# Kernel tuning notes

Hardware: AMD Instinct MI355X
Metric: run time of the kernel (lower is better)

## Reference

```python
import jax, jax.numpy as jnp
import numpy as np

NUM_NODES = 100000
EMB = 64
HID = 128
OUT = 64
N_EDGES = 1600000
N_LABEL = 200000


def setup_inputs() -> dict:
    key = jax.random.key(0)
    ks = jax.random.split(key, 8)
    return {
        "emb": jax.random.normal(ks[0], (NUM_NODES, EMB), jnp.float32) * 0.05,
        "w1l": jax.random.normal(ks[1], (HID, EMB), jnp.float32) * 0.05,
        "w1r": jax.random.normal(ks[2], (HID, EMB), jnp.float32) * 0.05,
        "b1": jnp.zeros((HID,), jnp.float32),
        "w2l": jax.random.normal(ks[3], (OUT, HID), jnp.float32) * 0.05,
        "w2r": jax.random.normal(ks[4], (OUT, HID), jnp.float32) * 0.05,
        "b2": jnp.zeros((OUT,), jnp.float32),
        "edge_index": jax.random.randint(ks[5], (2, N_EDGES), 0, NUM_NODES, jnp.int32),
        "edge_label_index": jax.random.randint(ks[6], (2, N_LABEL), 0, NUM_NODES, jnp.int32),
    }


def reference(emb, w1l, w1r, b1, w2l, w2r, b2, edge_index, edge_label_index):
    # PyG SAGEConv (aggr='mean'): out = mean_{j in N(i)} x_j @ W_l^T + b_l + x_i @ W_r^T
    n = emb.shape[0]
    src, dst = edge_index[0], edge_index[1]
    # in-degree per destination node, clamped to avoid div-by-zero (isolated nodes -> 0 agg)
    deg = jax.ops.segment_sum(jnp.ones(src.shape, emb.dtype), dst, num_segments=n)
    inv_deg = 1.0 / jnp.maximum(deg, 1.0)

    def sage(x, wl, wr, b):
        agg = jax.ops.segment_sum(x[src], dst, num_segments=n) * inv_deg[:, None]
        return agg @ wl.T + x @ wr.T + b

    h = jax.nn.relu(sage(emb, w1l, w1r, b1))  # dropout is identity in eval mode
    z = sage(h, w2l, w2r, b2)  # [N, OUT]
    # dot-product decode over candidate pairs
    return jnp.sum(z[edge_label_index[0]] * z[edge_label_index[1]], axis=-1)
```

## Files before the change

### kernel.cpp

```cpp
#include <hip/hip_runtime.h>

#define NN   100000
#define EMB  64
#define HID  128
#define OUTD 64
#define NE   1600000
#define NL   200000
#define NBUK 6250
#define NG   8
#define CAPG 128
#define BSTR 6272

#define BUK_BLOCKS  1563
#define CEMB_BLOCKS 400
#define CW_BLOCKS   64

typedef __attribute__((ext_vector_type(4))) float f32x4;
typedef __attribute__((ext_vector_type(8))) short s16x8;
typedef __attribute__((ext_vector_type(4))) unsigned short us4;
typedef __attribute__((ext_vector_type(4))) int v4i;

__device__ __forceinline__ unsigned short f2bf(float f) {
    unsigned u = __float_as_uint(f);
    u += 0x7FFFu + ((u >> 16) & 1u);
    return (unsigned short)(u >> 16);
}
__device__ __forceinline__ float bf2f(unsigned short h) {
    return __uint_as_float(((unsigned)h) << 16);
}

__device__ __forceinline__ unsigned xcc_id() {
    unsigned v;
    asm volatile("s_getreg_b32 %0, hwreg(HW_REG_XCC_ID)" : "=s"(v));
    return v & (NG - 1);
}

__global__ void __launch_bounds__(256) prep_kernel(
        const int* __restrict__ src, const int* __restrict__ dst,
        int* __restrict__ bcnt, int* __restrict__ tmp,
        const float* __restrict__ emb, unsigned short* __restrict__ embb,
        const float* __restrict__ w1l, const float* __restrict__ w1r,
        const float* __restrict__ w2l, const float* __restrict__ w2r,
        unsigned short* __restrict__ w1cat, unsigned short* __restrict__ w2cat) {
    const int bid = blockIdx.x;
    const int tid = threadIdx.x;

    if (bid < BUK_BLOCKS) {
        int i = bid * 256 + tid;
        if (i >= NE / 4) return;
        unsigned g = xcc_id();
        int* cb = bcnt + g * BSTR;
        v4i d4 = __builtin_nontemporal_load((const v4i*)dst + i);
        v4i s4 = __builtin_nontemporal_load((const v4i*)src + i);
        int b0 = d4[0] >> 4, b1 = d4[1] >> 4, b2 = d4[2] >> 4, b3 = d4[3] >> 4;
        int p0 = atomicAdd(&cb[b0], 1);
        int p1 = atomicAdd(&cb[b1], 1);
        int p2 = atomicAdd(&cb[b2], 1);
        int p3 = atomicAdd(&cb[b3], 1);
        if (p0 < CAPG) tmp[((size_t)g * NBUK + b0) * CAPG + p0] = ((d4[0] & 15) << 17) | s4[0];
        if (p1 < CAPG) tmp[((size_t)g * NBUK + b1) * CAPG + p1] = ((d4[1] & 15) << 17) | s4[1];
        if (p2 < CAPG) tmp[((size_t)g * NBUK + b2) * CAPG + p2] = ((d4[2] & 15) << 17) | s4[2];
        if (p3 < CAPG) tmp[((size_t)g * NBUK + b3) * CAPG + p3] = ((d4[3] & 15) << 17) | s4[3];
    } else if (bid < BUK_BLOCKS + CEMB_BLOCKS) {
        for (int i = (bid - BUK_BLOCKS) * 256 + tid; i < NN * 16; i += CEMB_BLOCKS * 256) {
            float4 v = ((const float4*)emb)[i];
            us4 o;
            o.x = f2bf(v.x); o.y = f2bf(v.y); o.z = f2bf(v.z); o.w = f2bf(v.w);
            ((us4*)embb)[i] = o;
        }
    } else {
        int t = (bid - BUK_BLOCKS - CEMB_BLOCKS) * 256 + tid;
        if (t >= 128 * 128) return;
        int o = t >> 7, k = t & 127;
        w1cat[t] = f2bf(k < 64 ? w1l[o * 64 + k] : w1r[o * 64 + (k - 64)]);
        w2cat[t] = f2bf(o < 64 ? w2l[o * 128 + k] : w2r[(o - 64) * 128 + k]);
    }
}

template<bool L1>
__global__ void __launch_bounds__(256) agg16_kernel(
        const int* __restrict__ bcnt, const int* __restrict__ tmp,
        const unsigned short* __restrict__ xb,
        const float* __restrict__ hz, const float* __restrict__ bias,
        unsigned short* __restrict__ outb) {
    __shared__ int cgs[NG];
    __shared__ int goff[NG];
    __shared__ int total;
    __shared__ int scnt[16];
    __shared__ int soff[16];
    __shared__ int scur[16];
    __shared__ int plist[NG * CAPG];
    __shared__ int slist[NG * CAPG];

    const int b    = blockIdx.x;
    const int tid  = threadIdx.x;
    const int lane = tid & 63;
    const int wv   = tid >> 6;

    if (tid < NG) cgs[tid] = min(bcnt[tid * BSTR + b], CAPG);
    if (tid < 16) scnt[tid] = 0;
    __syncthreads();

    if (tid == 0) {
        int acc = 0;
#pragma unroll
        for (int g = 0; g < NG; ++g) { int c = cgs[g]; goff[g] = acc; acc += c; }
        total = acc;
    }
    __syncthreads();

    for (int t = tid; t < NG * CAPG; t += 256) {
        int g = t >> 7;
        int i = t & (CAPG - 1);
        if (i < cgs[g])
            plist[goff[g] + i] = __builtin_nontemporal_load(
                tmp + ((size_t)g * NBUK + b) * CAPG + i);
    }
    __syncthreads();

    const int cnt = total;
    for (int i = tid; i < cnt; i += 256)
        atomicAdd(&scnt[plist[i] >> 17], 1);
    __syncthreads();

    if (tid == 0) {
        int acc = 0;
#pragma unroll
        for (int r = 0; r < 16; ++r) {
            soff[r] = acc;
            scur[r] = acc;
            acc += scnt[r];
        }
    }
    __syncthreads();

    for (int i = tid; i < cnt; i += 256) {
        int p = plist[i];
        int pos = atomicAdd(&scur[p >> 17], 1);
        slist[pos] = p & 0x1FFFF;
    }
    __syncthreads();

#define LDX(c) bf2f(xb[(size_t)(c) * 64 + lane])
    for (int r = wv; r < 16; r += 4) {
        const int node = b * 16 + r;
        const int s = soff[r];
        const int d = scnt[r];
        float acc = 0.f;
        int j = 0;
        for (; j + 8 <= d; j += 8) {
            int c0 = slist[s + j + 0], c1 = slist[s + j + 1];
            int c2 = slist[s + j + 2], c3 = slist[s + j + 3];
            int c4 = slist[s + j + 4], c5 = slist[s + j + 5];
            int c6 = slist[s + j + 6], c7 = slist[s + j + 7];
            float v0 = LDX(c0), v1 = LDX(c1), v2 = LDX(c2), v3 = LDX(c3);
            float v4 = LDX(c4), v5 = LDX(c5), v6 = LDX(c6), v7 = LDX(c7);
            acc += ((v0 + v1) + (v2 + v3)) + ((v4 + v5) + (v6 + v7));
        }
        if (j + 4 <= d) {
            int c0 = slist[s + j + 0], c1 = slist[s + j + 1];
            int c2 = slist[s + j + 2], c3 = slist[s + j + 3];
            float v0 = LDX(c0), v1 = LDX(c1), v2 = LDX(c2), v3 = LDX(c3);
            acc += (v0 + v1) + (v2 + v3);
            j += 4;
        }
        for (; j < d; ++j) acc += LDX(slist[s + j]);

        const float inv = 1.0f / fmaxf((float)d, 1.0f);
        if (L1) {
            outb[(size_t)node * 64 + lane] = f2bf(acc * inv);
        } else {
            outb[(size_t)node * 64 + lane] =
                f2bf(acc * inv + hz[(size_t)node * 64 + lane] + bias[lane]);
        }
    }
#undef LDX
}

__global__ void __launch_bounds__(256) gemm_mfma_kernel(
        const unsigned short* __restrict__ aggb, const unsigned short* __restrict__ embb,
        const unsigned short* __restrict__ w1cat, const float* __restrict__ b1,
        const unsigned short* __restrict__ w2cat,
        unsigned short* __restrict__ p2b, float* __restrict__ hz) {
    __shared__ unsigned short h_lds[128 * 136];

    const int tid  = threadIdx.x;
    const int lane = tid & 63;
    const int w    = tid >> 6;
    const int l15  = lane & 15;
    const int lk   = lane >> 4;
    const int n_base = blockIdx.x * 128;
    const int mrow0  = w * 32;

    f32x4 acc[2][8];
#pragma unroll
    for (int mt = 0; mt < 2; ++mt)
#pragma unroll
        for (int nt = 0; nt < 8; ++nt) acc[mt][nt] = (f32x4)(0.f);

#pragma unroll
    for (int ks = 0; ks < 4; ++ks) {
        const int kc = ks * 32 + lk * 8;
        s16x8 a[2];
#pragma unroll
        for (int mt = 0; mt < 2; ++mt) {
            int n = n_base + mrow0 + mt * 16 + l15;
            s16x8 av = (s16x8)(short)0;
            if (n < NN) {
                const unsigned short* ap = (kc < 64)
                    ? (aggb + (size_t)n * 64 + kc)
                    : (embb + (size_t)n * 64 + (kc - 64));
                av = *(const s16x8*)ap;
            }
            a[mt] = av;
        }
#pragma unroll
        for (int nt = 0; nt < 8; ++nt) {
            s16x8 bv = *(const s16x8*)(w1cat + (nt * 16 + l15) * 128 + kc);
            acc[0][nt] = __builtin_amdgcn_mfma_f32_16x16x32_bf16(a[0], bv, acc[0][nt], 0, 0, 0);
            acc[1][nt] = __builtin_amdgcn_mfma_f32_16x16x32_bf16(a[1], bv, acc[1][nt], 0, 0, 0);
        }
    }

    float b1v[8];
#pragma unroll
    for (int nt = 0; nt < 8; ++nt) b1v[nt] = b1[nt * 16 + l15];
#pragma unroll
    for (int mt = 0; mt < 2; ++mt)
#pragma unroll
        for (int nt = 0; nt < 8; ++nt) {
            f32x4 d = acc[mt][nt];
            int o = nt * 16 + l15;
            int r0 = mrow0 + mt * 16 + lk * 4;
#pragma unroll
            for (int j = 0; j < 4; ++j)
                h_lds[(r0 + j) * 136 + o] = f2bf(fmaxf(d[j] + b1v[nt], 0.f));
        }

#pragma unroll
    for (int mt = 0; mt < 2; ++mt)
#pragma unroll
        for (int nt = 0; nt < 8; ++nt) acc[mt][nt] = (f32x4)(0.f);

#pragma unroll
    for (int ks = 0; ks < 4; ++ks) {
        const int kc = ks * 32 + lk * 8;
        s16x8 a[2];
#pragma unroll
        for (int mt = 0; mt < 2; ++mt)
            a[mt] = *(const s16x8*)&h_lds[(mrow0 + mt * 16 + l15) * 136 + kc];
#pragma unroll
        for (int nt = 0; nt < 8; ++nt) {
            s16x8 bv = *(const s16x8*)(w2cat + (nt * 16 + l15) * 128 + kc);
            acc[0][nt] = __builtin_amdgcn_mfma_f32_16x16x32_bf16(a[0], bv, acc[0][nt], 0, 0, 0);
            acc[1][nt] = __builtin_amdgcn_mfma_f32_16x16x32_bf16(a[1], bv, acc[1][nt], 0, 0, 0);
        }
    }

#pragma unroll
    for (int mt = 0; mt < 2; ++mt)
#pragma unroll
        for (int nt = 0; nt < 8; ++nt) {
            f32x4 d = acc[mt][nt];
            int o = nt * 16 + l15;
            int r0 = n_base + mrow0 + mt * 16 + lk * 4;
#pragma unroll
            for (int j = 0; j < 4; ++j) {
                int r = r0 + j;
                if (r >= NN) continue;
                if (nt < 4) p2b[(size_t)r * 64 + o] = f2bf(d[j]);
                else        hz[(size_t)r * 64 + (o - 64)] = d[j];
            }
        }
}

__global__ void decode_kernel(const int* __restrict__ a, const int* __restrict__ b,
                              const unsigned short* __restrict__ zb, float* __restrict__ out) {
    int t = blockIdx.x * blockDim.x + threadIdx.x;
    int k = t >> 4;
    int q = t & 15;
    if (k >= NL) return;
    int ia = a[k], ib = b[k];
    us4 va = ((const us4*)zb)[ia * 16 + q];
    us4 vb = ((const us4*)zb)[ib * 16 + q];
    float s = bf2f(va.x) * bf2f(vb.x) + bf2f(va.y) * bf2f(vb.y)
            + bf2f(va.z) * bf2f(vb.z) + bf2f(va.w) * bf2f(vb.w);
    s += __shfl_xor(s, 1, 64);
    s += __shfl_xor(s, 2, 64);
    s += __shfl_xor(s, 4, 64);
    s += __shfl_xor(s, 8, 64);
    if (q == 0) out[k] = s;
}

extern "C" void kernel_launch(void* const* d_in, const int* in_sizes, int n_in,
                              void* d_out, int out_size, void* d_ws, size_t ws_size,
                              hipStream_t stream) {
    const float* emb = (const float*)d_in[0];
    const float* w1l = (const float*)d_in[1];
    const float* w1r = (const float*)d_in[2];
    const float* b1  = (const float*)d_in[3];
    const float* w2l = (const float*)d_in[4];
    const float* w2r = (const float*)d_in[5];
    const float* b2  = (const float*)d_in[6];
    const int*   ei  = (const int*)d_in[7];
    const int*   eli = (const int*)d_in[8];
    float* out = (float*)d_out;

    int* bcnt = (int*)d_ws;
    int* tmp  = bcnt + NG * BSTR;
    unsigned short* aggb  = (unsigned short*)(tmp + (size_t)NG * NBUK * CAPG);
    unsigned short* embb  = aggb + (size_t)NN * 64;
    unsigned short* p2b   = embb + (size_t)NN * 64;
    unsigned short* zb    = p2b + (size_t)NN * 64;
    unsigned short* w1cat = zb + (size_t)NN * 64;
    unsigned short* w2cat = w1cat + 128 * 128;
    float* hz = (float*)(w2cat + 128 * 128);

    const int* src = ei;
    const int* dst = ei + NE;

    hipMemsetAsync(bcnt, 0, (size_t)NG * BSTR * sizeof(int), stream);

    prep_kernel<<<BUK_BLOCKS + CEMB_BLOCKS + CW_BLOCKS, 256, 0, stream>>>(
        src, dst, bcnt, tmp, emb, embb, w1l, w1r, w2l, w2r, w1cat, w2cat);

    agg16_kernel<true><<<NBUK, 256, 0, stream>>>(bcnt, tmp, embb, nullptr, nullptr, aggb);

    const int NT = (NN + 127) / 128;
    gemm_mfma_kernel<<<NT, 256, 0, stream>>>(aggb, embb, w1cat, b1, w2cat, p2b, hz);

    agg16_kernel<false><<<NBUK, 256, 0, stream>>>(bcnt, tmp, p2b, hz, b2, zb);

    decode_kernel<<<(NL * 16 + 255) / 256, 256, 0, stream>>>(eli, eli + NL, zb, out);
}
```

Before: 233.8 us.

## Widen edge buckets from 16 to 128 destination nodes per aggregation block

Destination buckets now hold 128 nodes instead of 16, so there are 782 buckets with up to 512 edges per XCC group, and the aggregation kernel runs 512 threads (8 waves) per block. The aim is fewer, larger buckets: less atomic contention spread, fewer blocks and less per-block setup overhead in the aggregation. In exchange, the per-block LDS footprint grows, the single-thread 128-entry prefix scan is serial, and any bucket whose count exceeds the 512-entry cap drops edges. The expected count per group-bucket is about 256, so overflow is unlikely but not impossible. Nontemporal loads of the bucket data were also dropped.

```diff
diff --git a/kernel.cpp b/kernel.cpp
--- a/kernel.cpp
+++ b/kernel.cpp
@@ -6,10 +6,10 @@
 #define OUTD 64
 #define NE   1600000
 #define NL   200000
-#define NBUK 6250
+#define NBUK 782
 #define NG   8
-#define CAPG 128
-#define BSTR 6272
+#define CAPB 512
+#define BSTR 784
 
 #define BUK_BLOCKS  1563
 #define CEMB_BLOCKS 400
@@ -52,15 +52,16 @@
         int* cb = bcnt + g * BSTR;
         v4i d4 = __builtin_nontemporal_load((const v4i*)dst + i);
         v4i s4 = __builtin_nontemporal_load((const v4i*)src + i);
-        int b0 = d4[0] >> 4, b1 = d4[1] >> 4, b2 = d4[2] >> 4, b3 = d4[3] >> 4;
+        int b0 = d4[0] >> 7, b1 = d4[1] >> 7, b2 = d4[2] >> 7, b3 = d4[3] >> 7;
         int p0 = atomicAdd(&cb[b0], 1);
         int p1 = atomicAdd(&cb[b1], 1);
         int p2 = atomicAdd(&cb[b2], 1);
         int p3 = atomicAdd(&cb[b3], 1);
-        if (p0 < CAPG) tmp[((size_t)g * NBUK + b0) * CAPG + p0] = ((d4[0] & 15) << 17) | s4[0];
-        if (p1 < CAPG) tmp[((size_t)g * NBUK + b1) * CAPG + p1] = ((d4[1] & 15) << 17) | s4[1];
-        if (p2 < CAPG) tmp[((size_t)g * NBUK + b2) * CAPG + p2] = ((d4[2] & 15) << 17) | s4[2];
-        if (p3 < CAPG) tmp[((size_t)g * NBUK + b3) * CAPG + p3] = ((d4[3] & 15) << 17) | s4[3];
+        int* tg = tmp + ((size_t)g * NBUK << 9);
+        if (p0 < CAPB) tg[(b0 << 9) + p0] = ((d4[0] & 127) << 17) | s4[0];
+        if (p1 < CAPB) tg[(b1 << 9) + p1] = ((d4[1] & 127) << 17) | s4[1];
+        if (p2 < CAPB) tg[(b2 << 9) + p2] = ((d4[2] & 127) << 17) | s4[2];
+        if (p3 < CAPB) tg[(b3 << 9) + p3] = ((d4[3] & 127) << 17) | s4[3];
     } else if (bid < BUK_BLOCKS + CEMB_BLOCKS) {
         for (int i = (bid - BUK_BLOCKS) * 256 + tid; i < NN * 16; i += CEMB_BLOCKS * 256) {
             float4 v = ((const float4*)emb)[i];
@@ -78,7 +79,7 @@
 }
 
 template<bool L1>
-__global__ void __launch_bounds__(256) agg16_kernel(
+__global__ void __launch_bounds__(512) agg_kernel(
         const int* __restrict__ bcnt, const int* __restrict__ tmp,
         const unsigned short* __restrict__ xb,
         const float* __restrict__ hz, const float* __restrict__ bias,
@@ -86,19 +87,19 @@
     __shared__ int cgs[NG];
     __shared__ int goff[NG];
     __shared__ int total;
-    __shared__ int scnt[16];
-    __shared__ int soff[16];
-    __shared__ int scur[16];
-    __shared__ int plist[NG * CAPG];
-    __shared__ int slist[NG * CAPG];
+    __shared__ int scnt[128];
+    __shared__ int soff[128];
+    __shared__ int scur[128];
+    __shared__ int plist[NG * CAPB];
+    __shared__ int slist[NG * CAPB];
 
     const int b    = blockIdx.x;
     const int tid  = threadIdx.x;
     const int lane = tid & 63;
     const int wv   = tid >> 6;
 
-    if (tid < NG) cgs[tid] = min(bcnt[tid * BSTR + b], CAPG);
-    if (tid < 16) scnt[tid] = 0;
+    if (tid < NG) cgs[tid] = min(bcnt[tid * BSTR + b], CAPB);
+    if (tid < 128) scnt[tid] = 0;
     __syncthreads();
 
     if (tid == 0) {
@@ -109,24 +110,22 @@
     }
     __syncthreads();
 
-    for (int t = tid; t < NG * CAPG; t += 256) {
-        int g = t >> 7;
-        int i = t & (CAPG - 1);
+    for (int t = tid; t < NG * CAPB; t += 512) {
+        int g = t >> 9;
+        int i = t & (CAPB - 1);
         if (i < cgs[g])
-            plist[goff[g] + i] = __builtin_nontemporal_load(
-                tmp + ((size_t)g * NBUK + b) * CAPG + i);
+            plist[goff[g] + i] = tmp[(((size_t)g * NBUK + b) << 9) + i];
     }
     __syncthreads();
 
     const int cnt = total;
-    for (int i = tid; i < cnt; i += 256)
+    for (int i = tid; i < cnt; i += 512)
         atomicAdd(&scnt[plist[i] >> 17], 1);
     __syncthreads();
 
     if (tid == 0) {
         int acc = 0;
-#pragma unroll
-        for (int r = 0; r < 16; ++r) {
+        for (int r = 0; r < 128; ++r) {
             soff[r] = acc;
             scur[r] = acc;
             acc += scnt[r];
@@ -134,7 +133,7 @@
     }
     __syncthreads();
 
-    for (int i = tid; i < cnt; i += 256) {
+    for (int i = tid; i < cnt; i += 512) {
         int p = plist[i];
         int pos = atomicAdd(&scur[p >> 17], 1);
         slist[pos] = p & 0x1FFFF;
@@ -142,8 +141,9 @@
     __syncthreads();
 
 #define LDX(c) bf2f(xb[(size_t)(c) * 64 + lane])
-    for (int r = wv; r < 16; r += 4) {
-        const int node = b * 16 + r;
+    for (int r = wv; r < 128; r += 8) {
+        const int node = b * 128 + r;
+        if (node >= NN) continue;
         const int s = soff[r];
         const int d = scnt[r];
         float acc = 0.f;
@@ -308,7 +308,7 @@
 
     int* bcnt = (int*)d_ws;
     int* tmp  = bcnt + NG * BSTR;
-    unsigned short* aggb  = (unsigned short*)(tmp + (size_t)NG * NBUK * CAPG);
+    unsigned short* aggb  = (unsigned short*)(tmp + (size_t)NG * NBUK * CAPB);
     unsigned short* embb  = aggb + (size_t)NN * 64;
     unsigned short* p2b   = embb + (size_t)NN * 64;
     unsigned short* zb    = p2b + (size_t)NN * 64;
@@ -324,12 +324,12 @@
     prep_kernel<<<BUK_BLOCKS + CEMB_BLOCKS + CW_BLOCKS, 256, 0, stream>>>(
         src, dst, bcnt, tmp, emb, embb, w1l, w1r, w2l, w2r, w1cat, w2cat);
 
-    agg16_kernel<true><<<NBUK, 256, 0, stream>>>(bcnt, tmp, embb, nullptr, nullptr, aggb);
+    agg_kernel<true><<<NBUK, 512, 0, stream>>>(bcnt, tmp, embb, nullptr, nullptr, aggb);
 
     const int NT = (NN + 127) / 128;
     gemm_mfma_kernel<<<NT, 256, 0, stream>>>(aggb, embb, w1cat, b1, w2cat, p2b, hz);
 
-    agg16_kernel<false><<<NBUK, 256, 0, stream>>>(bcnt, tmp, p2b, hz, b2, zb);
+    agg_kernel<false><<<NBUK, 512, 0, stream>>>(bcnt, tmp, p2b, hz, b2, zb);
 
     decode_kernel<<<(NL * 16 + 255) / 256, 256, 0, stream>>>(eli, eli + NL, zb, out);
 }
```

Result: slower. 264.1 us (+13.0%).
